# Kernel optimization log

Measured on AMD Instinct MI355X. Metric: run time of the kernel, lower is better.

The kernel has to match this reference:

```python
import jax, jax.numpy as jnp
import numpy as np

NUM_HEADS = 2
LN_EPS = 1e-5
NEG_MASK = -1e9


def setup_inputs() -> dict:
    key = jax.random.key(0)
    ks = jax.random.split(key, 8)
    B, C, T, N = 8, 64, 32, 400
    H, D = NUM_HEADS, C // NUM_HEADS
    s = 1.0 / np.sqrt(C)
    return {
        "x": jax.random.normal(ks[0], (B, C, T, N), dtype=jnp.float32),
        "Wq": jax.random.normal(ks[1], (C, C), dtype=jnp.float32) * s,
        "Wk": jax.random.normal(ks[2], (C, C), dtype=jnp.float32) * s,
        "Wv": jax.random.normal(ks[3], (C, C), dtype=jnp.float32) * s,
        "a_src": jax.random.normal(ks[4], (H, D), dtype=jnp.float32) * 0.1,
        "a_dst": jax.random.normal(ks[5], (H, D), dtype=jnp.float32) * 0.1,
        "ln_gamma": jnp.ones((C,), dtype=jnp.float32),
        "ln_beta": jnp.zeros((C,), dtype=jnp.float32),
        "gso": jax.random.randint(ks[6], (N, N), 0, 2, dtype=jnp.int32),
    }


def reference(x, Wq, Wk, Wv, a_src, a_dst, ln_gamma, ln_beta, gso):
    B, C, T, N = x.shape
    H = NUM_HEADS
    D = C // H
    # (B,C,T,N) -> (B*T, N, C)
    xr = jnp.transpose(x, (0, 2, 3, 1)).reshape(B * T, N, C)
    # torch Linear: y = x @ W.T; then split heads -> (BT, N, H, D)
    Q = (xr @ Wq.T).reshape(B * T, N, H, D)
    K = (xr @ Wk.T).reshape(B * T, N, H, D)
    V = (xr @ Wv.T).reshape(B * T, N, H, D)
    # GAT additive scores per head
    s_src = jnp.einsum("bnhd,hd->bnh", Q, a_src)  # (BT, N, H)
    s_dst = jnp.einsum("bnhd,hd->bnh", K, a_dst)  # (BT, N, H)
    scores = s_src[:, :, None, :] + s_dst[:, None, :, :]  # (BT, i, j, H)
    scores = jax.nn.leaky_relu(scores, negative_slope=0.2)
    mask = jnp.where(gso == 0, jnp.float32(NEG_MASK), 0.0)  # (N, N)
    scores = scores + mask[None, :, :, None]
    attn = jax.nn.softmax(scores, axis=2)  # softmax over dst j; dropout = identity (eval)
    out = jnp.einsum("bijh,bjhd->bihd", attn, V).reshape(B * T, N, C)
    # LayerNorm over channel dim
    mu = jnp.mean(out, axis=-1, keepdims=True)
    var = jnp.var(out, axis=-1, keepdims=True)
    out = (out - mu) * jax.lax.rsqrt(var + LN_EPS) * ln_gamma + ln_beta
    # (BT, N, C) -> (B, C, T, N)
    return jnp.transpose(out.reshape(B, T, N, C), (0, 3, 1, 2))
```

## Files before the change

### kernel.cpp

```cpp
#include <hip/hip_runtime.h>
#include <hip/hip_bf16.h>

typedef __attribute__((ext_vector_type(8))) short bf16x8;
typedef __attribute__((ext_vector_type(4))) float f32x4;
typedef __attribute__((ext_vector_type(4))) int i32x4;
typedef __attribute__((ext_vector_type(4))) unsigned int u32x4;
typedef __attribute__((ext_vector_type(2))) unsigned int u32x2;

#define B_   8
#define C_   64
#define T_   32
#define N_   400
#define BT_  256
#define NKT_ 13
#define CN_  12800
#define VROW 424
#define WROW 72
#define L2E_ 1.4426950408889634f
#define SH6_ (-8.656170245333780f)

#if __has_builtin(__builtin_amdgcn_exp2f)
#define EXP2F(x) __builtin_amdgcn_exp2f(x)
#else
#define EXP2F(x) __expf((x) * 0.6931471805599453f)
#endif

#define BARRIER() asm volatile("s_waitcnt lgkmcnt(0)\n\ts_barrier" ::: "memory")

__global__ __launch_bounds__(256) void gat_prep(
    const int* __restrict__ gso, unsigned int* __restrict__ mb)
{
  int idx = blockIdx.x*256 + threadIdx.x;
  if (idx < N_*16) {
    int i = idx >> 4, kw = idx & 15;
    unsigned int bits = 0;
    if (kw < 13) {
      int j0 = kw * 32;
      #pragma unroll
      for (int bb = 0; bb < 32; ++bb) {
        int j = j0 + bb;
        if (j < N_ && gso[i*N_ + j] != 0) bits |= (1u << bb);
      }
    }
    mb[idx] = bits;
  }
}

__global__ __launch_bounds__(1024) void gat_fused(
    const float* __restrict__ x, const float* __restrict__ Wq,
    const float* __restrict__ Wk, const float* __restrict__ Wv,
    const float* __restrict__ a_src, const float* __restrict__ a_dst,
    const float* __restrict__ gamma, const float* __restrict__ beta,
    const unsigned int* __restrict__ mb, float* __restrict__ out)
{
  __shared__ __align__(16) __hip_bfloat16 Vt[64][VROW];
  __shared__ __align__(16) __hip_bfloat16 wvb[80][WROW];
  __shared__ __align__(16) float e1d_s[2][416];
  __shared__ __align__(16) float e2d_s[2][416];
  __shared__ __align__(16) float si_s[2][400];
  __shared__ __align__(16) float ob[128][68];
  __shared__ __align__(16) unsigned int lut_s[16][2];
  __shared__ float g_s[64], b_s[64];

  const int tid = threadIdx.x;
  const int bt = blockIdx.x;
  const int b = bt >> 5, t = bt & 31;
  const int lane = tid & 63, wave = tid >> 6;
  const int col = lane & 15, quad = lane >> 4;

  #pragma unroll
  for (int it = 0; it < 4; ++it) {
    int idx = it*1024 + tid;
    int o = idx >> 6, c = idx & 63;
    wvb[o][c] = __float2bfloat16(Wv[o*C_ + c]);
  }
  if (tid < 256) {
    int ww = tid >> 6, c = tid & 63, h = ww >> 1;
    const float* W = (ww & 1) ? Wk : Wq;
    const float* a = (ww & 1) ? a_dst : a_src;
    float s = 0.f;
    #pragma unroll
    for (int d = 0; d < 32; ++d) s += W[(h*32 + d)*C_ + c] * a[h*32 + d];
    wvb[64 + ww][c] = __float2bfloat16(s * L2E_);
  } else if (tid < 320) {
    g_s[tid - 256] = gamma[tid - 256];
  } else if (tid < 384) {
    b_s[tid - 320] = beta[tid - 320];
  } else if (tid < 448) {
    int tt = tid - 384;
    int h = (tt >> 4) & 1, cc = 400 + (tt & 15);
    if (tt < 32) e1d_s[h][cc] = 0.f; else e2d_s[h][cc] = 0.f;
  } else if (tid < 464) {
    int n = tid - 448;
    lut_s[n][0] = ((n & 1) ? 0x0000FFFFu : 0u) | ((n & 2) ? 0xFFFF0000u : 0u);
    lut_s[n][1] = ((n & 4) ? 0x0000FFFFu : 0u) | ((n & 8) ? 0xFFFF0000u : 0u);
  }
  for (int idx = tid; idx < 12*WROW; idx += 1024)
    wvb[68 + idx/WROW][idx % WROW] = __float2bfloat16(0.f);
  for (int idx = tid; idx < 64*24; idx += 1024)
    Vt[idx/24][400 + idx%24] = __float2bfloat16(0.f);
  BARRIER();

  {
    const float* xbase = x + ((size_t)b*C_*T_ + t)*N_;
    for (int nt = wave; nt < 25; nt += 16) {
      const int n0 = nt*16;
      bf16x8 bfrag[2];
      #pragma unroll
      for (int kt = 0; kt < 2; ++kt) {
        const float* xc = xbase + (size_t)(kt*32 + quad*8)*CN_ + n0 + col;
        union { short s[8]; bf16x8 v; } pk;
        #pragma unroll
        for (int j = 0; j < 8; ++j) {
          union { __hip_bfloat16 h; short s; } cv;
          cv.h = __float2bfloat16(xc[(size_t)j*CN_]);
          pk.s[j] = cv.s;
        }
        bfrag[kt] = pk.v;
      }
      #pragma unroll
      for (int ot = 0; ot < 5; ++ot) {
        f32x4 acc = {0.f, 0.f, 0.f, 0.f};
        #pragma unroll
        for (int kt = 0; kt < 2; ++kt) {
          bf16x8 afr = *(const bf16x8*)&wvb[ot*16 + col][kt*32 + quad*8];
          acc = __builtin_amdgcn_mfma_f32_16x16x32_bf16(afr, bfrag[kt], acc, 0, 0, 0);
        }
        if (ot < 4) {
          #pragma unroll
          for (int r = 0; r < 4; ++r)
            Vt[ot*16 + quad*4 + r][n0 + col] = __float2bfloat16(acc[r]);
        } else if (quad == 0) {
          #pragma unroll
          for (int r = 0; r < 4; ++r) {
            int h = r >> 1;
            if (r & 1) {
              e1d_s[h][n0 + col] = EXP2F(acc[r] + SH6_);
              e2d_s[h][n0 + col] = EXP2F(fmaf(0.2f, acc[r], SH6_));
            } else {
              si_s[h][n0 + col] = acc[r];
            }
          }
        }
      }
    }
  }
  BARRIER();

  const int hh = wave & 1, itile = wave >> 1;
  const int rowA = col;
  const unsigned int qsh = quad * 8;

  bf16x8 ones;
  #pragma unroll
  for (int k = 0; k < 8; ++k) ones[k] = (short)0x3F80;

  for (int r0 = 0; r0 < N_; r0 += 128) {
    const int ibase = r0 + itile*16;
    if (ibase < N_) {
      const int irow = ibase + rowA;
      const float si1 = si_s[hh][irow];
      const float E1i = EXP2F(si1 + SH6_);
      const float E2i = EXP2F(fmaf(0.2f, si1, SH6_));
      const u32x4* mp = (const u32x4*)(mb + irow*16);
      u32x4 mw0 = mp[0], mw1 = mp[1], mw2 = mp[2];
      unsigned int mw12 = mb[irow*16 + 12];
      const float* e1p = e1d_s[hh] + quad*8;
      const float* e2p = e2d_s[hh] + quad*8;
      const __hip_bfloat16* v0p = &Vt[hh*32 + rowA][quad*8];
      const __hip_bfloat16* v1p = v0p + 16*VROW;

      f32x4 d0 = {0,0,0,0}, d1 = {0,0,0,0}, d2 = {0,0,0,0};
      #pragma unroll
      for (int kt = 0; kt < NKT_; ++kt) {
        unsigned int mword = (kt < 4) ? mw0[kt] : (kt < 8) ? mw1[kt-4]
                           : (kt < 12) ? mw2[kt-8] : mw12;
        unsigned int mbyte = (mword >> qsh) & 0xffu;
        u32x2 mlo = *(const u32x2*)&lut_s[mbyte & 15u][0];
        u32x2 mhi = *(const u32x2*)&lut_s[mbyte >> 4][0];
        f32x4 x1a = *(const f32x4*)(e1p + kt*32);
        f32x4 x1b = *(const f32x4*)(e1p + kt*32 + 4);
        f32x4 x2a = *(const f32x4*)(e2p + kt*32);
        f32x4 x2b = *(const f32x4*)(e2p + kt*32 + 4);
        bf16x8 vb0 = *(const bf16x8*)(v0p + kt*32);
        bf16x8 vb1 = *(const bf16x8*)(v1p + kt*32);
        unsigned int eu[8];
        #pragma unroll
        for (int jj = 0; jj < 8; ++jj) {
          float f1 = (jj < 4) ? x1a[jj] : x1b[jj-4];
          float f2 = (jj < 4) ? x2a[jj] : x2b[jj-4];
          eu[jj] = __float_as_uint(fmaxf(E1i * f1, E2i * f2));
        }
        union { i32x4 i; bf16x8 v; } af;
        af.i.x = (int)(__builtin_amdgcn_perm(eu[1], eu[0], 0x07060302u) & mlo.x);
        af.i.y = (int)(__builtin_amdgcn_perm(eu[3], eu[2], 0x07060302u) & mlo.y);
        af.i.z = (int)(__builtin_amdgcn_perm(eu[5], eu[4], 0x07060302u) & mhi.x);
        af.i.w = (int)(__builtin_amdgcn_perm(eu[7], eu[6], 0x07060302u) & mhi.y);
        d0 = __builtin_amdgcn_mfma_f32_16x16x32_bf16(af.v, vb0, d0, 0, 0, 0);
        d1 = __builtin_amdgcn_mfma_f32_16x16x32_bf16(af.v, vb1, d1, 0, 0, 0);
        d2 = __builtin_amdgcn_mfma_f32_16x16x32_bf16(af.v, ones, d2, 0, 0, 0);
      }
      #pragma unroll
      for (int r = 0; r < 4; ++r) {
        float li = 1.0f / d2[r];
        int rl = itile*16 + quad*4 + r;
        ob[rl][hh*32 + rowA]      = d0[r] * li;
        ob[rl][hh*32 + 16 + rowA] = d1[r] * li;
      }
    }
    BARRIER();

    {
      int rl = tid >> 3, cgi = tid & 7;
      int n = r0 + rl;
      if (n < N_) {
        float u[8]; float s = 0.f;
        #pragma unroll
        for (int k = 0; k < 8; ++k) { u[k] = ob[rl][cgi*8 + k]; s += u[k]; }
        s += __shfl_xor(s,1); s += __shfl_xor(s,2); s += __shfl_xor(s,4);
        float mu = s * (1.f/64.f);
        float q = 0.f;
        #pragma unroll
        for (int k = 0; k < 8; ++k) { float dv = u[k]-mu; q = fmaf(dv,dv,q); }
        q += __shfl_xor(q,1); q += __shfl_xor(q,2); q += __shfl_xor(q,4);
        float rstd = rsqrtf(q*(1.f/64.f) + 1e-5f);
        #pragma unroll
        for (int k = 0; k < 8; ++k)
          ob[rl][cgi*8 + k] = (u[k]-mu)*rstd*g_s[cgi*8 + k] + b_s[cgi*8 + k];
      }
    }
    BARRIER();

    #pragma unroll
    for (int it = 0; it < 8; ++it) {
      int idx = it*1024 + tid;
      int c = idx >> 7, nn = idx & 127;
      int n = r0 + nn;
      if (n < N_) out[((size_t)(b*C_ + c)*T_ + t)*N_ + n] = ob[nn][c];
    }
    BARRIER();
  }
}

extern "C" void kernel_launch(void* const* d_in, const int* in_sizes, int n_in,
                              void* d_out, int out_size, void* d_ws, size_t ws_size,
                              hipStream_t stream) {
  (void)in_sizes; (void)n_in; (void)out_size; (void)ws_size;
  const float* x     = (const float*)d_in[0];
  const float* Wq    = (const float*)d_in[1];
  const float* Wk    = (const float*)d_in[2];
  const float* Wv    = (const float*)d_in[3];
  const float* a_src = (const float*)d_in[4];
  const float* a_dst = (const float*)d_in[5];
  const float* gamma = (const float*)d_in[6];
  const float* beta  = (const float*)d_in[7];
  const int*   gso   = (const int*)d_in[8];
  float* out = (float*)d_out;

  unsigned int* mbp = (unsigned int*)d_ws;

  gat_prep<<<26, 256, 0, stream>>>(gso, mbp);
  gat_fused<<<BT_, 1024, 0, stream>>>(x, Wq, Wk, Wv, a_src, a_dst,
                                      gamma, beta, mbp, out);
}
```

Baseline: 116.5 us.

## Split each (b,t) slice across two 512-thread blocks and alias LDS buffers

Launches 512 blocks of 512 threads, each handling half of the 400 query rows for one (b,t) slice, instead of 256 blocks of 1024 threads. Each block still recomputes the full V projection and score vectors for its slice. The Wv staging buffer and the output staging buffer now share one LDS region, and the V row pitch is trimmed, to cut LDS use so more blocks fit per CU. This aims to fill the GPU's CUs better and improve occupancy, at the cost of doing the projection work twice per slice.

```diff
diff --git a/kernel.cpp b/kernel.cpp
--- a/kernel.cpp
+++ b/kernel.cpp
@@ -11,11 +11,12 @@
 #define C_   64
 #define T_   32
 #define N_   400
-#define BT_  256
 #define NKT_ 13
 #define CN_  12800
-#define VROW 424
+#define VROW 416
 #define WROW 72
+#define OBW  65
+#define IROWS 200
 #define L2E_ 1.4426950408889634f
 #define SH6_ (-8.656170245333780f)
 
@@ -46,7 +47,7 @@
   }
 }
 
-__global__ __launch_bounds__(1024) void gat_fused(
+__global__ __launch_bounds__(512, 4) void gat_fused(
     const float* __restrict__ x, const float* __restrict__ Wq,
     const float* __restrict__ Wk, const float* __restrict__ Wv,
     const float* __restrict__ a_src, const float* __restrict__ a_dst,
@@ -54,23 +55,26 @@
     const unsigned int* __restrict__ mb, float* __restrict__ out)
 {
   __shared__ __align__(16) __hip_bfloat16 Vt[64][VROW];
-  __shared__ __align__(16) __hip_bfloat16 wvb[80][WROW];
+  __shared__ __align__(16) unsigned char uni[64*OBW*4];
   __shared__ __align__(16) float e1d_s[2][416];
   __shared__ __align__(16) float e2d_s[2][416];
   __shared__ __align__(16) float si_s[2][400];
-  __shared__ __align__(16) float ob[128][68];
   __shared__ __align__(16) unsigned int lut_s[16][2];
   __shared__ float g_s[64], b_s[64];
 
+  auto wvb = (__hip_bfloat16 (*)[WROW])uni;
+  auto ob  = (float (*)[OBW])uni;
+
   const int tid = threadIdx.x;
-  const int bt = blockIdx.x;
+  const int bt = blockIdx.x >> 1, io = blockIdx.x & 1;
   const int b = bt >> 5, t = bt & 31;
+  const int i0 = io * IROWS;
   const int lane = tid & 63, wave = tid >> 6;
   const int col = lane & 15, quad = lane >> 4;
 
   #pragma unroll
-  for (int it = 0; it < 4; ++it) {
-    int idx = it*1024 + tid;
+  for (int it = 0; it < 8; ++it) {
+    int idx = it*512 + tid;
     int o = idx >> 6, c = idx & 63;
     wvb[o][c] = __float2bfloat16(Wv[o*C_ + c]);
   }
@@ -95,15 +99,17 @@
     lut_s[n][0] = ((n & 1) ? 0x0000FFFFu : 0u) | ((n & 2) ? 0xFFFF0000u : 0u);
     lut_s[n][1] = ((n & 4) ? 0x0000FFFFu : 0u) | ((n & 8) ? 0xFFFF0000u : 0u);
   }
-  for (int idx = tid; idx < 12*WROW; idx += 1024)
+  for (int idx = tid; idx < 12*WROW; idx += 512)
     wvb[68 + idx/WROW][idx % WROW] = __float2bfloat16(0.f);
-  for (int idx = tid; idx < 64*24; idx += 1024)
-    Vt[idx/24][400 + idx%24] = __float2bfloat16(0.f);
+  { int r = tid >> 3, c = tid & 7;
+    Vt[r][400 + c] = __float2bfloat16(0.f); }
+  for (int idx = tid; idx < 64*8; idx += 512)
+    Vt[idx >> 3][408 + (idx & 7)] = __float2bfloat16(0.f);
   BARRIER();
 
   {
     const float* xbase = x + ((size_t)b*C_*T_ + t)*N_;
-    for (int nt = wave; nt < 25; nt += 16) {
+    for (int nt = wave; nt < 25; nt += 8) {
       const int n0 = nt*16;
       bf16x8 bfrag[2];
       #pragma unroll
@@ -155,20 +161,24 @@
   #pragma unroll
   for (int k = 0; k < 8; ++k) ones[k] = (short)0x3F80;
 
-  for (int r0 = 0; r0 < N_; r0 += 128) {
-    const int ibase = r0 + itile*16;
-    if (ibase < N_) {
-      const int irow = ibase + rowA;
+  const float* e1p = e1d_s[hh] + quad*8;
+  const float* e2p = e2d_s[hh] + quad*8;
+  const __hip_bfloat16* v0p = &Vt[hh*32 + rowA][quad*8];
+  const __hip_bfloat16* v1p = v0p + 16*VROW;
+
+  for (int p = 0; p < 4; ++p) {
+    const int r0 = p*64;
+    const int ibl = r0 + itile*16;
+    if (ibl < IROWS) {
+      const int lrow = ibl + rowA;
+      const bool lv = lrow < IROWS;
+      const int irow = i0 + (lv ? lrow : 0);
       const float si1 = si_s[hh][irow];
-      const float E1i = EXP2F(si1 + SH6_);
-      const float E2i = EXP2F(fmaf(0.2f, si1, SH6_));
+      const float E1i = lv ? EXP2F(si1 + SH6_) : 0.f;
+      const float E2i = lv ? EXP2F(fmaf(0.2f, si1, SH6_)) : 0.f;
       const u32x4* mp = (const u32x4*)(mb + irow*16);
       u32x4 mw0 = mp[0], mw1 = mp[1], mw2 = mp[2];
       unsigned int mw12 = mb[irow*16 + 12];
-      const float* e1p = e1d_s[hh] + quad*8;
-      const float* e2p = e2d_s[hh] + quad*8;
-      const __hip_bfloat16* v0p = &Vt[hh*32 + rowA][quad*8];
-      const __hip_bfloat16* v1p = v0p + 16*VROW;
 
       f32x4 d0 = {0,0,0,0}, d1 = {0,0,0,0}, d2 = {0,0,0,0};
       #pragma unroll
@@ -202,18 +212,19 @@
       }
       #pragma unroll
       for (int r = 0; r < 4; ++r) {
-        float li = 1.0f / d2[r];
-        int rl = itile*16 + quad*4 + r;
-        ob[rl][hh*32 + rowA]      = d0[r] * li;
-        ob[rl][hh*32 + 16 + rowA] = d1[r] * li;
+        int rj = itile*16 + quad*4 + r;
+        if (r0 + rj < IROWS) {
+          float li = 1.0f / d2[r];
+          ob[rj][hh*32 + rowA]      = d0[r] * li;
+          ob[rj][hh*32 + 16 + rowA] = d1[r] * li;
+        }
       }
     }
     BARRIER();
 
     {
       int rl = tid >> 3, cgi = tid & 7;
-      int n = r0 + rl;
-      if (n < N_) {
+      if (r0 + rl < IROWS) {
         float u[8]; float s = 0.f;
         #pragma unroll
         for (int k = 0; k < 8; ++k) { u[k] = ob[rl][cgi*8 + k]; s += u[k]; }
@@ -233,10 +244,10 @@
 
     #pragma unroll
     for (int it = 0; it < 8; ++it) {
-      int idx = it*1024 + tid;
-      int c = idx >> 7, nn = idx & 127;
-      int n = r0 + nn;
-      if (n < N_) out[((size_t)(b*C_ + c)*T_ + t)*N_ + n] = ob[nn][c];
+      int idx = it*512 + tid;
+      int c = idx >> 6, nn = idx & 63;
+      if (r0 + nn < IROWS)
+        out[((size_t)(b*C_ + c)*T_ + t)*N_ + i0 + r0 + nn] = ob[nn][c];
     }
     BARRIER();
   }
@@ -260,6 +271,6 @@
   unsigned int* mbp = (unsigned int*)d_ws;
 
   gat_prep<<<26, 256, 0, stream>>>(gso, mbp);
-  gat_fused<<<BT_, 1024, 0, stream>>>(x, Wq, Wk, Wv, a_src, a_dst,
-                                      gamma, beta, mbp, out);
+  gat_fused<<<512, 512, 0, stream>>>(x, Wq, Wk, Wv, a_src, a_dst,
+                                     gamma, beta, mbp, out);
 }
```

Result: slower. 120.7 us (+3.7%).
